# Kernel tuning notes

Measured on AMD Instinct MI355X. Metric: run time of the kernel, lower is better.

The kernel has to match this reference:

```python
import jax, jax.numpy as jnp
import numpy as np

D_MODEL = 768
D_STATE = 16
D_CONV = 4
EXPAND = 2
D_INNER = EXPAND * D_MODEL
DT_RANK = (D_MODEL + 15) // 16  # 48
BATCH = 2
SEQ = 1024
LN_EPS = 1e-5


def setup_inputs() -> dict:
    key = jax.random.key(0)
    ks = jax.random.split(key, 12)
    s = 0.02
    inp = {
        "x": jax.random.normal(ks[0], (BATCH, SEQ, D_MODEL), dtype=jnp.float32),
        "in_proj_w": jax.random.normal(ks[1], (2 * D_INNER, D_MODEL), dtype=jnp.float32) * s,
        "conv_w": jax.random.normal(ks[2], (D_INNER, D_CONV), dtype=jnp.float32) * s,
        "conv_b": jnp.zeros((D_INNER,), dtype=jnp.float32),
        "x_proj_w": jax.random.normal(ks[3], (DT_RANK + 2 * D_STATE, D_INNER), dtype=jnp.float32) * s,
        "dt_proj_w": jax.random.normal(ks[4], (D_INNER, DT_RANK), dtype=jnp.float32) * s,
        "dt_proj_b": jnp.full((D_INNER,), -4.0, dtype=jnp.float32),  # softplus(-4) ~ small dt
        "A_log": jnp.log(jnp.broadcast_to(jnp.arange(1, D_STATE + 1, dtype=jnp.float32), (D_INNER, D_STATE))),
        "D": jnp.ones((D_INNER,), dtype=jnp.float32),
        "out_proj_w": jax.random.normal(ks[5], (D_MODEL, D_INNER), dtype=jnp.float32) * s,
        "ln_w": jnp.ones((D_MODEL,), dtype=jnp.float32),
        "ln_b": jnp.zeros((D_MODEL,), dtype=jnp.float32),
    }
    return inp


def _mamba(x, in_proj_w, conv_w, conv_b, x_proj_w, dt_proj_w, dt_proj_b, A_log, D, out_proj_w):
    B, L, _ = x.shape
    # input projection -> [B, L, 2*D_INNER], split into x-branch and gate z
    xz = jnp.einsum("bld,ed->ble", x, in_proj_w)
    xb, z = jnp.split(xz, 2, axis=-1)
    # causal depthwise conv1d along L
    lhs = jnp.transpose(xb, (0, 2, 1))  # [B, D_INNER, L]
    rhs = conv_w[:, None, :]  # [D_INNER, 1, D_CONV]
    xc = jax.lax.conv_general_dilated(
        lhs, rhs, window_strides=(1,), padding=[(D_CONV - 1, 0)],
        dimension_numbers=("NCH", "OIH", "NCH"), feature_group_count=D_INNER)
    xc = jnp.transpose(xc, (0, 2, 1)) + conv_b  # [B, L, D_INNER]
    xc = jax.nn.silu(xc)
    # data-dependent SSM parameters
    x_dbl = jnp.einsum("bld,ed->ble", xc, x_proj_w)  # [B, L, DT_RANK+2*D_STATE]
    dt, Bm, Cm = jnp.split(x_dbl, [DT_RANK, DT_RANK + D_STATE], axis=-1)
    dt = jax.nn.softplus(jnp.einsum("blr,dr->bld", dt, dt_proj_w) + dt_proj_b)  # [B, L, D_INNER]
    A = -jnp.exp(A_log)  # [D_INNER, D_STATE]

    # selective scan over time
    def step(h, inp):
        dt_t, B_t, C_t, u_t = inp  # [B,D_INNER], [B,D_STATE], [B,D_STATE], [B,D_INNER]
        dA = jnp.exp(dt_t[:, :, None] * A)  # [B, D_INNER, D_STATE]
        h = h * dA + (dt_t * u_t)[:, :, None] * B_t[:, None, :]
        y = jnp.einsum("bds,bs->bd", h, C_t)
        return h, y

    h0 = jnp.zeros((B, D_INNER, D_STATE), dtype=x.dtype)
    xs = (jnp.transpose(dt, (1, 0, 2)), jnp.transpose(Bm, (1, 0, 2)),
          jnp.transpose(Cm, (1, 0, 2)), jnp.transpose(xc, (1, 0, 2)))
    _, ys = jax.lax.scan(step, h0, xs)  # ys: [L, B, D_INNER]
    y = jnp.transpose(ys, (1, 0, 2)) + xc * D
    y = y * jax.nn.silu(z)
    return jnp.einsum("ble,de->bld", y, out_proj_w)  # [B, L, D_MODEL]


def reference(x, in_proj_w, conv_w, conv_b, x_proj_w, dt_proj_w, dt_proj_b,
              A_log, D, out_proj_w, ln_w, ln_b):
    residual = x
    h = _mamba(x, in_proj_w, conv_w, conv_b, x_proj_w, dt_proj_w, dt_proj_b, A_log, D, out_proj_w)
    # dropout is identity in eval mode
    y = h + residual
    mu = jnp.mean(y, axis=-1, keepdims=True)
    var = jnp.mean(jnp.square(y - mu), axis=-1, keepdims=True)
    return (y - mu) * jax.lax.rsqrt(var + LN_EPS) * ln_w + ln_b
```

## Files before the change

### kernel.cpp

```cpp
#include <hip/hip_runtime.h>
#include <hip/hip_bf16.h>
#include <math.h>

#define BATCH   2
#define SEQ     1024
#define DMODEL  768
#define DINNER  1536
#define DSTATE  16
#define DTRANK  48
#define NTOK    (BATCH*SEQ)
#define XPROJ_N (DTRANK + 2*DSTATE)

#define LC      32
#define NC      (SEQ/LC)

typedef unsigned short ushort_t;
typedef __attribute__((ext_vector_type(8))) short bf16x8;
typedef __attribute__((ext_vector_type(4))) float f32x4;

__device__ __forceinline__ ushort_t f2bf(float f) {
    unsigned int u = __float_as_uint(f);
    u += 0x7FFF + ((u >> 16) & 1);
    return (ushort_t)(u >> 16);
}

__global__ __launch_bounds__(256)
void f2b_3(const float* __restrict__ s0, ushort_t* __restrict__ d0, int n0,
           const float* __restrict__ s1, ushort_t* __restrict__ d1, int n1,
           const float* __restrict__ s2, ushort_t* __restrict__ d2, int n2)
{
    const int i = (blockIdx.x * 256 + threadIdx.x) * 4;
    const float* s; ushort_t* d;
    if (i < n0)               { s = s0 + i;            d = d0 + i; }
    else if (i < n0 + n1)     { s = s1 + (i - n0);     d = d1 + (i - n0); }
    else if (i < n0 + n1 + n2){ s = s2 + (i - n0 - n1);d = d2 + (i - n0 - n1); }
    else return;
    const float4 v = *reinterpret_cast<const float4*>(s);
    ushort4 o;
    o.x = f2bf(v.x); o.y = f2bf(v.y); o.z = f2bf(v.z); o.w = f2bf(v.w);
    *reinterpret_cast<ushort4*>(d) = o;
}

#define GLOAD_LDS16(gp, lp) \
    __builtin_amdgcn_global_load_lds((const __attribute__((address_space(1))) void*)(gp), \
                                     (__attribute__((address_space(3))) void*)(lp), 16, 0, 0)

__global__ __launch_bounds__(256)
void gemm_mfma_bt(const ushort_t* __restrict__ A, const ushort_t* __restrict__ W,
                  float* __restrict__ C, int M, int N, int K)
{
    __shared__ ushort_t As[128 * 32];
    __shared__ ushort_t Bs[128 * 32];

    const int tid  = threadIdx.x;
    const int w    = tid >> 6;
    const int lane = tid & 63;
    const int m0 = blockIdx.y * 128;
    const int n0 = blockIdx.x * 128;

    const int lrow = lane >> 2;
    const int lcol = (lane & 3) * 8;

    const ushort_t* ga0 = A + (size_t)(m0 + w * 16 + lrow) * K + lcol;
    const ushort_t* ga1 = ga0 + (size_t)64 * K;
    const ushort_t* gb0 = W + (size_t)(n0 + w * 16 + lrow) * K + lcol;
    const ushort_t* gb1 = gb0 + (size_t)64 * K;

    ushort_t* lA0 = As + w * 512;
    ushort_t* lA1 = As + 64 * 32 + w * 512;
    ushort_t* lB0 = Bs + w * 512;
    ushort_t* lB1 = Bs + 64 * 32 + w * 512;

    const int wm = w >> 1, wn = w & 1;
    const int fr = lane & 15;
    const int kg = lane >> 4;

    f32x4 acc[4][4] = {};

    for (int kt = 0; kt < K; kt += 32) {
        __syncthreads();
        GLOAD_LDS16(ga0 + kt, lA0);
        GLOAD_LDS16(ga1 + kt, lA1);
        GLOAD_LDS16(gb0 + kt, lB0);
        GLOAD_LDS16(gb1 + kt, lB1);
        __syncthreads();

        bf16x8 af[4], bfr[4];
        #pragma unroll
        for (int i = 0; i < 4; ++i) {
            af[i]  = *reinterpret_cast<const bf16x8*>(&As[(wm * 64 + i * 16 + fr) * 32 + kg * 8]);
            bfr[i] = *reinterpret_cast<const bf16x8*>(&Bs[(wn * 64 + i * 16 + fr) * 32 + kg * 8]);
        }
        #pragma unroll
        for (int i = 0; i < 4; ++i)
            #pragma unroll
            for (int j = 0; j < 4; ++j)
                acc[i][j] = __builtin_amdgcn_mfma_f32_16x16x32_bf16(af[i], bfr[j], acc[i][j], 0, 0, 0);
    }

    #pragma unroll
    for (int i = 0; i < 4; ++i) {
        const int row_base = m0 + wm * 64 + i * 16 + kg * 4;
        #pragma unroll
        for (int j = 0; j < 4; ++j) {
            const int col = n0 + wn * 64 + j * 16 + fr;
            #pragma unroll
            for (int r = 0; r < 4; ++r)
                C[(size_t)(row_base + r) * N + col] = acc[i][j][r];
        }
    }
}

#define BM 64
#define BN 64
#define BK 16

template<int ACT>
__global__ __launch_bounds__(256)
void gemm_tn(const float* __restrict__ A, const float* __restrict__ W,
             const float* __restrict__ bias, float* __restrict__ C,
             int M, int N, int K, int lda)
{
    __shared__ float As[BK][BM + 4];
    __shared__ float Ws[BK][BN + 4];

    const int t  = threadIdx.x;
    const int tx = t & 15;
    const int ty = t >> 4;
    const int row0 = blockIdx.y * BM;
    const int col0 = blockIdx.x * BN;

    const int m_l = t >> 2;
    const int k_l = (t & 3) * 4;

    float acc[4][4] = {};

    for (int kt = 0; kt < K; kt += BK) {
        float4 av, wv;
        {
            const float* ap = A + (size_t)(row0 + m_l) * lda + kt + k_l;
            av = *reinterpret_cast<const float4*>(ap);
        }
        {
            const int wn = col0 + m_l;
            if (wn < N) {
                const float* wp = W + (size_t)wn * K + kt + k_l;
                wv = *reinterpret_cast<const float4*>(wp);
            } else {
                wv = make_float4(0.f, 0.f, 0.f, 0.f);
            }
        }
        __syncthreads();
        As[k_l + 0][m_l] = av.x; As[k_l + 1][m_l] = av.y;
        As[k_l + 2][m_l] = av.z; As[k_l + 3][m_l] = av.w;
        Ws[k_l + 0][m_l] = wv.x; Ws[k_l + 1][m_l] = wv.y;
        Ws[k_l + 2][m_l] = wv.z; Ws[k_l + 3][m_l] = wv.w;
        __syncthreads();

        #pragma unroll
        for (int k = 0; k < BK; ++k) {
            float4 a4 = *reinterpret_cast<const float4*>(&As[k][ty * 4]);
            float4 w4 = *reinterpret_cast<const float4*>(&Ws[k][tx * 4]);
            float af[4] = {a4.x, a4.y, a4.z, a4.w};
            float wf[4] = {w4.x, w4.y, w4.z, w4.w};
            #pragma unroll
            for (int i = 0; i < 4; ++i)
                #pragma unroll
                for (int j = 0; j < 4; ++j)
                    acc[i][j] += af[i] * wf[j];
        }
    }

    #pragma unroll
    for (int i = 0; i < 4; ++i) {
        const int m = row0 + ty * 4 + i;
        #pragma unroll
        for (int j = 0; j < 4; ++j) {
            const int n = col0 + tx * 4 + j;
            if (n < N) {
                float v = acc[i][j];
                if (ACT == 1) {
                    v += bias[n];
                    v = (v > 20.f) ? v : log1pf(expf(v));
                }
                C[(size_t)m * N + n] = v;
            }
        }
    }
}

__global__ __launch_bounds__(256)
void gemm_tn_splitk(const float* __restrict__ A, const float* __restrict__ W,
                    float* __restrict__ C, int M, int N, int K, int lda, int kchunk)
{
    __shared__ float As[BK][BM + 4];
    __shared__ float Ws[BK][BN + 4];

    const int t  = threadIdx.x;
    const int tx = t & 15;
    const int ty = t >> 4;
    const int row0 = blockIdx.y * BM;
    const int col0 = blockIdx.x * BN;
    const int kbeg = blockIdx.z * kchunk;
    const int kend = kbeg + kchunk;

    const int m_l = t >> 2;
    const int k_l = (t & 3) * 4;

    float acc[4][4] = {};

    for (int kt = kbeg; kt < kend; kt += BK) {
        float4 av, wv;
        {
            const float* ap = A + (size_t)(row0 + m_l) * lda + kt + k_l;
            av = *reinterpret_cast<const float4*>(ap);
        }
        {
            const int wn = col0 + m_l;
            if (wn < N) {
                const float* wp = W + (size_t)wn * K + kt + k_l;
                wv = *reinterpret_cast<const float4*>(wp);
            } else {
                wv = make_float4(0.f, 0.f, 0.f, 0.f);
            }
        }
        __syncthreads();
        As[k_l + 0][m_l] = av.x; As[k_l + 1][m_l] = av.y;
        As[k_l + 2][m_l] = av.z; As[k_l + 3][m_l] = av.w;
        Ws[k_l + 0][m_l] = wv.x; Ws[k_l + 1][m_l] = wv.y;
        Ws[k_l + 2][m_l] = wv.z; Ws[k_l + 3][m_l] = wv.w;
        __syncthreads();

        #pragma unroll
        for (int k = 0; k < BK; ++k) {
            float4 a4 = *reinterpret_cast<const float4*>(&As[k][ty * 4]);
            float4 w4 = *reinterpret_cast<const float4*>(&Ws[k][tx * 4]);
            float af[4] = {a4.x, a4.y, a4.z, a4.w};
            float wf[4] = {w4.x, w4.y, w4.z, w4.w};
            #pragma unroll
            for (int i = 0; i < 4; ++i)
                #pragma unroll
                for (int j = 0; j < 4; ++j)
                    acc[i][j] += af[i] * wf[j];
        }
    }

    #pragma unroll
    for (int i = 0; i < 4; ++i) {
        const int m = row0 + ty * 4 + i;
        #pragma unroll
        for (int j = 0; j < 4; ++j) {
            const int n = col0 + tx * 4 + j;
            if (n < N)
                atomicAdd(&C[(size_t)m * N + n], acc[i][j]);
        }
    }
}

__global__ __launch_bounds__(256)
void conv_silu(const float* __restrict__ xz, const float* __restrict__ cw,
               const float* __restrict__ cb, float* __restrict__ xc)
{
    int idx = blockIdx.x * 256 + threadIdx.x;
    if (idx >= NTOK * DINNER) return;
    const int c = idx % DINNER;
    const int m = idx / DINNER;
    const int l = m & (SEQ - 1);

    const float w0 = cw[c * 4 + 0], w1 = cw[c * 4 + 1],
                w2 = cw[c * 4 + 2], w3 = cw[c * 4 + 3];
    const float* base = xz + (size_t)m * (2 * DINNER) + c;

    float acc = cb[c] + base[0] * w3;
    if (l >= 1) acc += base[-(2 * DINNER)]     * w2;
    if (l >= 2) acc += base[-2 * (2 * DINNER)] * w1;
    if (l >= 3) acc += base[-3 * (2 * DINNER)] * w0;

    const float sig = 1.f / (1.f + __expf(-acc));
    xc[idx] = acc * sig;
}

__global__ __launch_bounds__(256)
void scan_chunk_state(const float* __restrict__ dt, const float* __restrict__ xc,
                      const float* __restrict__ xdbl, const float* __restrict__ A_log,
                      float* __restrict__ hA, float* __restrict__ aP)
{
    __shared__ float B_s[LC * 16];

    const int c  = blockIdx.x;
    const int d0 = blockIdx.y * 256;
    const int b  = blockIdx.z;
    const int t  = threadIdx.x;
    const int d  = d0 + t;

    const size_t row0 = (size_t)b * SEQ + (size_t)c * LC;

    #pragma unroll
    for (int p = 0; p < (LC * 16) / 256; ++p) {
        const int idx = p * 256 + t;
        const int l = idx >> 4, j = idx & 15;
        B_s[idx] = xdbl[(row0 + l) * XPROJ_N + DTRANK + j];
    }
    __syncthreads();

    float Aval[16];
    #pragma unroll
    for (int q = 0; q < 4; ++q) {
        const float4 a4 = *reinterpret_cast<const float4*>(&A_log[(size_t)d * DSTATE + q * 4]);
        Aval[q*4+0] = -expf(a4.x); Aval[q*4+1] = -expf(a4.y);
        Aval[q*4+2] = -expf(a4.z); Aval[q*4+3] = -expf(a4.w);
    }

    float h[16];
    #pragma unroll
    for (int s = 0; s < 16; ++s) h[s] = 0.f;
    float dts = 0.f;

    #pragma unroll 2
    for (int l = 0; l < LC; ++l) {
        const size_t m = row0 + l;
        const float dtv = dt[m * DINNER + d];
        const float u   = xc[m * DINNER + d];
        const float du  = dtv * u;
        dts += dtv;
        float Bv[16];
        #pragma unroll
        for (int q = 0; q < 4; ++q) {
            const float4 b4 = *reinterpret_cast<const float4*>(&B_s[l * 16 + q * 4]);
            Bv[q*4+0] = b4.x; Bv[q*4+1] = b4.y; Bv[q*4+2] = b4.z; Bv[q*4+3] = b4.w;
        }
        #pragma unroll
        for (int s = 0; s < 16; ++s)
            h[s] = h[s] * __expf(dtv * Aval[s]) + du * Bv[s];
    }

    const size_t o = (((size_t)(b * NC + c) * DINNER) + d) * DSTATE;
    #pragma unroll
    for (int q = 0; q < 4; ++q) {
        float4 hv = make_float4(h[q*4+0], h[q*4+1], h[q*4+2], h[q*4+3]);
        float4 pv = make_float4(__expf(Aval[q*4+0]*dts), __expf(Aval[q*4+1]*dts),
                                __expf(Aval[q*4+2]*dts), __expf(Aval[q*4+3]*dts));
        *reinterpret_cast<float4*>(&hA[o + q*4]) = hv;
        *reinterpret_cast<float4*>(&aP[o + q*4]) = pv;
    }
}

__global__ __launch_bounds__(256)
void scan_combine(float* __restrict__ hA, const float* __restrict__ aP)
{
    const int idx = blockIdx.x * 256 + threadIdx.x;
    const int b  = idx / (DINNER * DSTATE);
    const int ds = idx % (DINNER * DSTATE);

    float h = 0.f;
    #pragma unroll
    for (int c = 0; c < NC; ++c) {
        const size_t o = ((size_t)(b * NC + c) * DINNER * DSTATE) + ds;
        const float a = hA[o];
        const float p = aP[o];
        hA[o] = h;
        h = a + h * p;
    }
}

__global__ __launch_bounds__(256)
void scan_apply(const float* __restrict__ dt, const float* __restrict__ xc,
                const float* __restrict__ xdbl, const float* __restrict__ xz,
                const float* __restrict__ A_log, const float* __restrict__ Dp,
                const float* __restrict__ hInit, ushort_t* __restrict__ y)
{
    __shared__ float B_s[LC * 16];
    __shared__ float C_s[LC * 16];

    const int c  = blockIdx.x;
    const int d0 = blockIdx.y * 256;
    const int b  = blockIdx.z;
    const int t  = threadIdx.x;
    const int d  = d0 + t;

    const size_t row0 = (size_t)b * SEQ + (size_t)c * LC;

    #pragma unroll
    for (int p = 0; p < (LC * 16) / 256; ++p) {
        const int idx = p * 256 + t;
        const int l = idx >> 4, j = idx & 15;
        B_s[idx] = xdbl[(row0 + l) * XPROJ_N + DTRANK + j];
        C_s[idx] = xdbl[(row0 + l) * XPROJ_N + DTRANK + DSTATE + j];
    }
    __syncthreads();

    float Aval[16];
    #pragma unroll
    for (int q = 0; q < 4; ++q) {
        const float4 a4 = *reinterpret_cast<const float4*>(&A_log[(size_t)d * DSTATE + q * 4]);
        Aval[q*4+0] = -expf(a4.x); Aval[q*4+1] = -expf(a4.y);
        Aval[q*4+2] = -expf(a4.z); Aval[q*4+3] = -expf(a4.w);
    }
    const float Dd = Dp[d];

    const size_t o = (((size_t)(b * NC + c) * DINNER) + d) * DSTATE;
    float h[16];
    #pragma unroll
    for (int q = 0; q < 4; ++q) {
        const float4 h4 = *reinterpret_cast<const float4*>(&hInit[o + q*4]);
        h[q*4+0] = h4.x; h[q*4+1] = h4.y; h[q*4+2] = h4.z; h[q*4+3] = h4.w;
    }

    #pragma unroll 2
    for (int l = 0; l < LC; ++l) {
        const size_t m = row0 + l;
        const float dtv = dt[m * DINNER + d];
        const float u   = xc[m * DINNER + d];
        const float zv  = xz[m * (2 * DINNER) + DINNER + d];
        const float du  = dtv * u;

        float acc = 0.f;
        #pragma unroll
        for (int q = 0; q < 4; ++q) {
            const float4 b4 = *reinterpret_cast<const float4*>(&B_s[l * 16 + q * 4]);
            const float4 c4 = *reinterpret_cast<const float4*>(&C_s[l * 16 + q * 4]);
            const float bb[4] = {b4.x, b4.y, b4.z, b4.w};
            const float cc[4] = {c4.x, c4.y, c4.z, c4.w};
            #pragma unroll
            for (int r = 0; r < 4; ++r) {
                const int s = q * 4 + r;
                h[s] = h[s] * __expf(dtv * Aval[s]) + du * bb[r];
                acc += h[s] * cc[r];
            }
        }

        const float yv  = acc + u * Dd;
        const float sig = 1.f / (1.f + __expf(-zv));
        y[m * DINNER + d] = f2bf(yv * zv * sig);
    }
}

__global__ __launch_bounds__(256)
void ln_kernel(const float* __restrict__ mo, const float* __restrict__ x,
               const float* __restrict__ w, const float* __restrict__ bias,
               float* __restrict__ out)
{
    const int m = blockIdx.x;
    const int t = threadIdx.x;
    const float* mrow = mo + (size_t)m * DMODEL;
    const float* xrow = x  + (size_t)m * DMODEL;

    float v[3];
    float sum = 0.f, ss = 0.f;
    #pragma unroll
    for (int i = 0; i < 3; ++i) {
        const int col = t + 256 * i;
        v[i] = mrow[col] + xrow[col];
        sum += v[i];
        ss  += v[i] * v[i];
    }
    #pragma unroll
    for (int o = 1; o < 64; o <<= 1) {
        sum += __shfl_xor(sum, o);
        ss  += __shfl_xor(ss, o);
    }
    __shared__ float red[2][4];
    const int wid = t >> 6;
    if ((t & 63) == 0) { red[0][wid] = sum; red[1][wid] = ss; }
    __syncthreads();
    sum = red[0][0] + red[0][1] + red[0][2] + red[0][3];
    ss  = red[1][0] + red[1][1] + red[1][2] + red[1][3];

    const float mu   = sum * (1.f / DMODEL);
    const float var  = ss * (1.f / DMODEL) - mu * mu;
    const float rstd = rsqrtf(var + 1e-5f);

    #pragma unroll
    for (int i = 0; i < 3; ++i) {
        const int col = t + 256 * i;
        out[(size_t)m * DMODEL + col] = (v[i] - mu) * rstd * w[col] + bias[col];
    }
}

extern "C" void kernel_launch(void* const* d_in, const int* in_sizes, int n_in,
                              void* d_out, int out_size, void* d_ws, size_t ws_size,
                              hipStream_t stream)
{
    const float* x          = (const float*)d_in[0];
    const float* in_proj_w  = (const float*)d_in[1];
    const float* conv_w     = (const float*)d_in[2];
    const float* conv_b     = (const float*)d_in[3];
    const float* x_proj_w   = (const float*)d_in[4];
    const float* dt_proj_w  = (const float*)d_in[5];
    const float* dt_proj_b  = (const float*)d_in[6];
    const float* A_log      = (const float*)d_in[7];
    const float* Dp         = (const float*)d_in[8];
    const float* out_proj_w = (const float*)d_in[9];
    const float* ln_w       = (const float*)d_in[10];
    const float* ln_b       = (const float*)d_in[11];
    float* out = (float*)d_out;

    float* ws   = (float*)d_ws;
    float* xz   = ws;
    float* xc   = xz   + (size_t)NTOK * 3072;
    float* xdbl = xc   + (size_t)NTOK * 1536;
    float* dt   = xdbl + (size_t)NTOK * 80;
    float* mo   = dt   + (size_t)NTOK * 1536;
    ushort_t* xb16 = (ushort_t*)(mo + (size_t)NTOK * 768);
    ushort_t* ipw16 = xb16  + (size_t)NTOK * DMODEL;
    ushort_t* opw16 = ipw16 + (size_t)2 * DINNER * DMODEL;
    ushort_t* ybb   = opw16 + (size_t)DMODEL * DINNER;

    float* aP = mo;
    float* hA = (float*)d_out;

    {
        const int n0 = NTOK * DMODEL;
        const int n1 = 2 * DINNER * DMODEL;
        const int n2 = DMODEL * DINNER;
        const int nvec = (n0 + n1 + n2) / 4;
        f2b_3<<<(nvec + 255) / 256, 256, 0, stream>>>(
            x, xb16, n0, in_proj_w, ipw16, n1, out_proj_w, opw16, n2);
    }

    gemm_mfma_bt<<<dim3(2 * DINNER / 128, NTOK / 128), 256, 0, stream>>>(
        xb16, ipw16, xz, NTOK, 2 * DINNER, DMODEL);

    conv_silu<<<(NTOK * DINNER) / 256, 256, 0, stream>>>(xz, conv_w, conv_b, xc);

    hipMemsetAsync(xdbl, 0, (size_t)NTOK * XPROJ_N * sizeof(float), stream);
    gemm_tn_splitk<<<dim3((XPROJ_N + BN - 1) / BN, NTOK / BM, 8), 256, 0, stream>>>(
        xc, x_proj_w, xdbl, NTOK, XPROJ_N, DINNER, DINNER, DINNER / 8);

    gemm_tn<1><<<dim3(DINNER / BN, NTOK / BM), 256, 0, stream>>>(
        xdbl, dt_proj_w, dt_proj_b, dt, NTOK, DINNER, DTRANK, XPROJ_N);

    scan_chunk_state<<<dim3(NC, DINNER / 256, BATCH), 256, 0, stream>>>(
        dt, xc, xdbl, A_log, hA, aP);
    scan_combine<<<(BATCH * DINNER * DSTATE) / 256, 256, 0, stream>>>(hA, aP);
    scan_apply<<<dim3(NC, DINNER / 256, BATCH), 256, 0, stream>>>(
        dt, xc, xdbl, xz, A_log, Dp, hA, ybb);

    gemm_mfma_bt<<<dim3(DMODEL / 128, NTOK / 128), 256, 0, stream>>>(
        ybb, opw16, mo, NTOK, DMODEL, DINNER);

    ln_kernel<<<NTOK, 256, 0, stream>>>(mo, x, ln_w, ln_b, out);
}
```

Measured before the change: 274.6 us.

## Split-K the in_proj and out_proj MFMA GEMMs, reducing partials in consumers

Adds a split-K dimension to the bf16 MFMA GEMM. Each K-slice writes its own fp32 partial buffer, so no atomics are needed. The in_proj partials (2 slices) are summed inside conv_silu and scan_apply, and the out_proj partials (4 slices) are summed inside the layernorm kernel. The goal is to fill more CUs, especially for the small 96-block out_proj launch. The cost is extra global traffic to write and reread the partial buffers, and a larger workspace.

Result: faster. 257.1 us (-6.3%).

```diff
diff --git a/kernel.cpp b/kernel.cpp
--- a/kernel.cpp
+++ b/kernel.cpp
@@ -13,6 +13,9 @@
 
 #define LC      32
 #define NC      (SEQ/LC)
+
+#define KSPL_IN   2
+#define KSPL_OUT  4
 
 typedef unsigned short ushort_t;
 typedef __attribute__((ext_vector_type(8))) short bf16x8;
@@ -46,8 +49,8 @@
                                      (__attribute__((address_space(3))) void*)(lp), 16, 0, 0)
 
 __global__ __launch_bounds__(256)
-void gemm_mfma_bt(const ushort_t* __restrict__ A, const ushort_t* __restrict__ W,
-                  float* __restrict__ C, int M, int N, int K)
+void gemm_mfma_bt_sk(const ushort_t* __restrict__ A, const ushort_t* __restrict__ W,
+                     float* __restrict__ C, int M, int N, int K, int klen)
 {
     __shared__ ushort_t As[128 * 32];
     __shared__ ushort_t Bs[128 * 32];
@@ -57,13 +60,15 @@
     const int lane = tid & 63;
     const int m0 = blockIdx.y * 128;
     const int n0 = blockIdx.x * 128;
+    const int kbeg = blockIdx.z * klen;
+    float* Cp = C + (size_t)blockIdx.z * M * N;
 
     const int lrow = lane >> 2;
     const int lcol = (lane & 3) * 8;
 
-    const ushort_t* ga0 = A + (size_t)(m0 + w * 16 + lrow) * K + lcol;
+    const ushort_t* ga0 = A + (size_t)(m0 + w * 16 + lrow) * K + kbeg + lcol;
     const ushort_t* ga1 = ga0 + (size_t)64 * K;
-    const ushort_t* gb0 = W + (size_t)(n0 + w * 16 + lrow) * K + lcol;
+    const ushort_t* gb0 = W + (size_t)(n0 + w * 16 + lrow) * K + kbeg + lcol;
     const ushort_t* gb1 = gb0 + (size_t)64 * K;
 
     ushort_t* lA0 = As + w * 512;
@@ -77,7 +82,7 @@
 
     f32x4 acc[4][4] = {};
 
-    for (int kt = 0; kt < K; kt += 32) {
+    for (int kt = 0; kt < klen; kt += 32) {
         __syncthreads();
         GLOAD_LDS16(ga0 + kt, lA0);
         GLOAD_LDS16(ga1 + kt, lA1);
@@ -106,7 +111,7 @@
             const int col = n0 + wn * 64 + j * 16 + fr;
             #pragma unroll
             for (int r = 0; r < 4; ++r)
-                C[(size_t)(row_base + r) * N + col] = acc[i][j][r];
+                Cp[(size_t)(row_base + r) * N + col] = acc[i][j][r];
         }
     }
 }
@@ -258,8 +263,9 @@
 }
 
 __global__ __launch_bounds__(256)
-void conv_silu(const float* __restrict__ xz, const float* __restrict__ cw,
-               const float* __restrict__ cb, float* __restrict__ xc)
+void conv_silu(const float* __restrict__ xzA, const float* __restrict__ xzB,
+               const float* __restrict__ cw, const float* __restrict__ cb,
+               float* __restrict__ xc)
 {
     int idx = blockIdx.x * 256 + threadIdx.x;
     if (idx >= NTOK * DINNER) return;
@@ -269,12 +275,14 @@
 
     const float w0 = cw[c * 4 + 0], w1 = cw[c * 4 + 1],
                 w2 = cw[c * 4 + 2], w3 = cw[c * 4 + 3];
-    const float* base = xz + (size_t)m * (2 * DINNER) + c;
-
-    float acc = cb[c] + base[0] * w3;
-    if (l >= 1) acc += base[-(2 * DINNER)]     * w2;
-    if (l >= 2) acc += base[-2 * (2 * DINNER)] * w1;
-    if (l >= 3) acc += base[-3 * (2 * DINNER)] * w0;
+    const float* a = xzA + (size_t)m * (2 * DINNER) + c;
+    const float* b = xzB + (size_t)m * (2 * DINNER) + c;
+    const int R = 2 * DINNER;
+
+    float acc = cb[c] + (a[0] + b[0]) * w3;
+    if (l >= 1) acc += (a[-R]     + b[-R])     * w2;
+    if (l >= 2) acc += (a[-2 * R] + b[-2 * R]) * w1;
+    if (l >= 3) acc += (a[-3 * R] + b[-3 * R]) * w0;
 
     const float sig = 1.f / (1.f + __expf(-acc));
     xc[idx] = acc * sig;
@@ -365,7 +373,8 @@
 
 __global__ __launch_bounds__(256)
 void scan_apply(const float* __restrict__ dt, const float* __restrict__ xc,
-                const float* __restrict__ xdbl, const float* __restrict__ xz,
+                const float* __restrict__ xdbl,
+                const float* __restrict__ xzA, const float* __restrict__ xzB,
                 const float* __restrict__ A_log, const float* __restrict__ Dp,
                 const float* __restrict__ hInit, ushort_t* __restrict__ y)
 {
@@ -411,7 +420,8 @@
         const size_t m = row0 + l;
         const float dtv = dt[m * DINNER + d];
         const float u   = xc[m * DINNER + d];
-        const float zv  = xz[m * (2 * DINNER) + DINNER + d];
+        const size_t zi = m * (2 * DINNER) + DINNER + d;
+        const float zv  = xzA[zi] + xzB[zi];
         const float du  = dtv * u;
 
         float acc = 0.f;
@@ -442,6 +452,7 @@
 {
     const int m = blockIdx.x;
     const int t = threadIdx.x;
+    const size_t MN = (size_t)NTOK * DMODEL;
     const float* mrow = mo + (size_t)m * DMODEL;
     const float* xrow = x  + (size_t)m * DMODEL;
 
@@ -450,9 +461,13 @@
     #pragma unroll
     for (int i = 0; i < 3; ++i) {
         const int col = t + 256 * i;
-        v[i] = mrow[col] + xrow[col];
-        sum += v[i];
-        ss  += v[i] * v[i];
+        float acc = xrow[col];
+        #pragma unroll
+        for (int p = 0; p < KSPL_OUT; ++p)
+            acc += mrow[p * MN + col];
+        v[i] = acc;
+        sum += acc;
+        ss  += acc * acc;
     }
     #pragma unroll
     for (int o = 1; o < 64; o <<= 1) {
@@ -497,14 +512,17 @@
 
     float* ws   = (float*)d_ws;
     float* xz   = ws;
-    float* xc   = xz   + (size_t)NTOK * 3072;
+    float* xc   = xz   + (size_t)KSPL_IN * NTOK * 3072;
     float* xdbl = xc   + (size_t)NTOK * 1536;
     float* dt   = xdbl + (size_t)NTOK * 80;
     float* mo   = dt   + (size_t)NTOK * 1536;
-    ushort_t* xb16 = (ushort_t*)(mo + (size_t)NTOK * 768);
+    ushort_t* xb16 = (ushort_t*)(mo + (size_t)KSPL_OUT * NTOK * 768);
     ushort_t* ipw16 = xb16  + (size_t)NTOK * DMODEL;
     ushort_t* opw16 = ipw16 + (size_t)2 * DINNER * DMODEL;
     ushort_t* ybb   = opw16 + (size_t)DMODEL * DINNER;
+
+    float* xzA = xz;
+    float* xzB = xz + (size_t)NTOK * 3072;
 
     float* aP = mo;
     float* hA = (float*)d_out;
@@ -518,10 +536,10 @@
             x, xb16, n0, in_proj_w, ipw16, n1, out_proj_w, opw16, n2);
     }
 
-    gemm_mfma_bt<<<dim3(2 * DINNER / 128, NTOK / 128), 256, 0, stream>>>(
-        xb16, ipw16, xz, NTOK, 2 * DINNER, DMODEL);
-
-    conv_silu<<<(NTOK * DINNER) / 256, 256, 0, stream>>>(xz, conv_w, conv_b, xc);
+    gemm_mfma_bt_sk<<<dim3(2 * DINNER / 128, NTOK / 128, KSPL_IN), 256, 0, stream>>>(
+        xb16, ipw16, xz, NTOK, 2 * DINNER, DMODEL, DMODEL / KSPL_IN);
+
+    conv_silu<<<(NTOK * DINNER) / 256, 256, 0, stream>>>(xzA, xzB, conv_w, conv_b, xc);
 
     hipMemsetAsync(xdbl, 0, (size_t)NTOK * XPROJ_N * sizeof(float), stream);
     gemm_tn_splitk<<<dim3((XPROJ_N + BN - 1) / BN, NTOK / BM, 8), 256, 0, stream>>>(
@@ -534,10 +552,10 @@
         dt, xc, xdbl, A_log, hA, aP);
     scan_combine<<<(BATCH * DINNER * DSTATE) / 256, 256, 0, stream>>>(hA, aP);
     scan_apply<<<dim3(NC, DINNER / 256, BATCH), 256, 0, stream>>>(
-        dt, xc, xdbl, xz, A_log, Dp, hA, ybb);
-
-    gemm_mfma_bt<<<dim3(DMODEL / 128, NTOK / 128), 256, 0, stream>>>(
-        ybb, opw16, mo, NTOK, DMODEL, DINNER);
+        dt, xc, xdbl, xzA, xzB, A_log, Dp, hA, ybb);
+
+    gemm_mfma_bt_sk<<<dim3(DMODEL / 128, NTOK / 128, KSPL_OUT), 256, 0, stream>>>(
+        ybb, opw16, mo, NTOK, DMODEL, DINNER, DINNER / KSPL_OUT);
 
     ln_kernel<<<NTOK, 256, 0, stream>>>(mo, x, ln_w, ln_b, out);
 }
```
